# Optimization experiments

Measured on AMD Instinct MI355X. Metric: run time of the kernel, lower is better.

The kernel has to match this reference:

```python
import jax, jax.numpy as jnp
import numpy as np

DIM = 1536
HEADS = 8
DK = 64            # key_size
DV = DIM // HEADS  # value_size = 192
NPF = 32           # num_rel_pos_features
LN_EPS = 1e-3


def central_mask_features(positions, features, seq_len):
    # Borzoi/baskerville central-mask positional basis
    pow_rate = jnp.exp(jnp.log(seq_len + 1.0) / features)
    center_widths = pow_rate ** jnp.arange(1, features + 1, dtype=jnp.float32)
    return (center_widths[None, :] > jnp.abs(positions)[:, None]).astype(jnp.float32)


def get_positional_embed(n, feature_size):
    distances = jnp.arange(-n + 1, n, dtype=jnp.float32)  # (2n-1,)
    emb = central_mask_features(distances, feature_size // 2, n)
    return jnp.concatenate([emb, jnp.sign(distances)[:, None] * emb], axis=-1)  # (2n-1, F)


def relative_shift(x):
    # x: (b, h, n, 2n-1) -> (b, h, n, n), Transformer-XL shift trick
    b, h, t1, t2 = x.shape
    x = jnp.pad(x, ((0, 0), (0, 0), (0, 0), (1, 0)))  # (b,h,n,2n)
    x = x.reshape(b, h, t2 + 1, t1)[:, :, 1:, :]       # (b,h,2n-1,n)
    x = x.reshape(b, h, t1, t2)
    return x[..., :((t2 + 1) // 2)]


def setup_inputs() -> dict:
    key = jax.random.key(0)
    ks = jax.random.split(key, 10)
    s = 0.02
    return {
        "x": jax.random.normal(ks[0], (1, 4096, DIM), jnp.float32),
        "ln_gamma": jnp.ones((DIM,), jnp.float32),
        "ln_beta": jnp.zeros((DIM,), jnp.float32),
        "Wq": jax.random.normal(ks[1], (DIM, HEADS * DK), jnp.float32) * s,
        "Wk": jax.random.normal(ks[2], (DIM, HEADS * DK), jnp.float32) * s,
        "Wv": jax.random.normal(ks[3], (DIM, HEADS * DV), jnp.float32) * s,
        "Wr": jax.random.normal(ks[4], (NPF, HEADS * DK), jnp.float32) * s,
        "Wo": jax.random.normal(ks[5], (HEADS * DV, DIM), jnp.float32) * s,
        "bo": jnp.zeros((DIM,), jnp.float32),
        "rel_content_bias": jax.random.normal(ks[6], (1, HEADS, 1, DK), jnp.float32),
        "rel_pos_bias": jax.random.normal(ks[7], (1, HEADS, 1, DK), jnp.float32),
    }


def reference(x, ln_gamma, ln_beta, Wq, Wk, Wv, Wr, Wo, bo, rel_content_bias, rel_pos_bias):
    B, N, D = x.shape
    # LayerNorm(eps=1e-3)
    mu = jnp.mean(x, axis=-1, keepdims=True)
    var = jnp.mean(jnp.square(x - mu), axis=-1, keepdims=True)
    xn = (x - mu) * jax.lax.rsqrt(var + LN_EPS) * ln_gamma + ln_beta
    # projections -> (B,H,N,d)
    q = (xn @ Wq).reshape(B, N, HEADS, DK).transpose(0, 2, 1, 3) * (DK ** -0.5)
    k = (xn @ Wk).reshape(B, N, HEADS, DK).transpose(0, 2, 1, 3)
    v = (xn @ Wv).reshape(B, N, HEADS, DV).transpose(0, 2, 1, 3)
    content_logits = jnp.einsum('bhid,bhjd->bhij', q + rel_content_bias, k)
    # relative positions (dropout is identity in eval mode)
    pos = get_positional_embed(N, NPF)                       # (2N-1, NPF)
    rel_k = (pos @ Wr).reshape(2 * N - 1, HEADS, DK).transpose(1, 0, 2)  # (H,2N-1,DK)
    rel_logits = jnp.einsum('bhid,hjd->bhij', q + rel_pos_bias, rel_k)   # (B,H,N,2N-1)
    rel_logits = relative_shift(rel_logits)                  # (B,H,N,N)
    attn = jax.nn.softmax(content_logits + rel_logits, axis=-1)
    out = jnp.einsum('bhij,bhjd->bhid', attn, v)
    out = out.transpose(0, 2, 1, 3).reshape(B, N, HEADS * DV)
    return out @ Wo + bo
```

## Files before the change

### kernel.cpp

```cpp
#include <hip/hip_runtime.h>
#include <hip/hip_bf16.h>
#include <math.h>

typedef __hip_bfloat16 bf16;
typedef __attribute__((ext_vector_type(8))) short bf16x8;
typedef __attribute__((ext_vector_type(4))) float f32x4;

#define DIMX 1536
#define NSEQ 4096
#define NHEAD 8
#define DKH 64
#define DVH 192
#define HDK 512
#define HDV 1536
#define KSPLIT 2
#define KVB 32

static __device__ __forceinline__ float b2f(bf16 x){ return __bfloat162float(x); }
static __device__ __forceinline__ bf16 f2b(float x){ return __float2bfloat16(x); }

#define GLD_TO_LDS(gsrc, ldst) __builtin_amdgcn_global_load_lds( \
    (const __attribute__((address_space(1))) unsigned int*)(gsrc), \
    (__attribute__((address_space(3))) unsigned int*)(ldst), 16, 0, 0)

__global__ __launch_bounds__(256) void k_cvtT(const float* __restrict__ W, bf16* __restrict__ WT, int K, int N){
  __shared__ float t[32][33];
  int n0 = blockIdx.x<<5, k0 = blockIdx.y<<5;
  int tx = threadIdx.x & 31, ty = threadIdx.x >> 5;
  #pragma unroll
  for (int r=ty; r<32; r+=8) t[r][tx] = W[(size_t)(k0+r)*N + n0 + tx];
  __syncthreads();
  #pragma unroll
  for (int r=ty; r<32; r+=8) WT[(size_t)(n0+r)*K + k0 + tx] = f2b(t[tx][r]);
}

__global__ __launch_bounds__(256) void k_cvtT2(const float* __restrict__ W, bf16* __restrict__ WTh,
                                               bf16* __restrict__ WTl, int K, int N){
  __shared__ float t[32][33];
  int n0 = blockIdx.x<<5, k0 = blockIdx.y<<5;
  int tx = threadIdx.x & 31, ty = threadIdx.x >> 5;
  #pragma unroll
  for (int r=ty; r<32; r+=8) t[r][tx] = W[(size_t)(k0+r)*N + n0 + tx];
  __syncthreads();
  #pragma unroll
  for (int r=ty; r<32; r+=8){
    float v = t[tx][r];
    bf16 hi = f2b(v);
    WTh[(size_t)(n0+r)*K + k0 + tx] = hi;
    WTl[(size_t)(n0+r)*K + k0 + tx] = f2b(v - b2f(hi));
  }
}

__global__ __launch_bounds__(256) void k_T(const bf16* __restrict__ src, bf16* __restrict__ dst, int R, int C){
  __shared__ bf16 t[64][65];
  int c0 = blockIdx.x<<6, r0 = blockIdx.y<<6;
  int tx = threadIdx.x & 63, ty = threadIdx.x >> 6;
  for (int r=ty; r<64; r+=4) t[r][tx] = src[(size_t)(r0+r)*C + c0 + tx];
  __syncthreads();
  for (int r=ty; r<64; r+=4){
    int dv = c0+r, kv = r0+tx;
    int kvp = (kv & ~31) | ((((kv>>3)&3) ^ (dv&3))<<3) | (kv&7);
    dst[(size_t)dv*R + kvp] = t[tx][r];
  }
}

__global__ __launch_bounds__(256) void k_ln(const float* __restrict__ x, const float* __restrict__ g,
                                            const float* __restrict__ b,
                                            bf16* __restrict__ xnh, bf16* __restrict__ xnl){
  int row = blockIdx.x, t = threadIdx.x;
  const float* xr = x + (size_t)row*DIMX;
  float v[6]; float s=0.f, ss=0.f;
  #pragma unroll
  for (int j=0;j<6;++j){ v[j]=xr[t+256*j]; s+=v[j]; ss+=v[j]*v[j]; }
  int lane = t&63, wave = t>>6;
  #pragma unroll
  for (int off=32; off>0; off>>=1){ s += __shfl_down(s,off,64); ss += __shfl_down(ss,off,64); }
  __shared__ float red[8];
  if (lane==0){ red[wave]=s; red[wave+4]=ss; }
  __syncthreads();
  s = red[0]+red[1]+red[2]+red[3];
  ss = red[4]+red[5]+red[6]+red[7];
  float mu = s*(1.f/DIMX);
  float var = ss*(1.f/DIMX) - mu*mu;
  float rstd = rsqrtf(var + 1e-3f);
  #pragma unroll
  for (int j=0;j<6;++j){
    int c = t+256*j;
    float xv = (v[j]-mu)*rstd*g[c] + b[c];
    bf16 hi = f2b(xv);
    xnh[(size_t)row*DIMX + c] = hi;
    xnl[(size_t)row*DIMX + c] = f2b(xv - b2f(hi));
  }
}

template<int EPI>
__global__ __launch_bounds__(256) void k_gemm(const bf16* __restrict__ A, const bf16* __restrict__ BT,
    void* __restrict__ Cout, const float* __restrict__ bias, int M, int N, int K)
{
  __shared__ bf16 As[128][32];
  __shared__ bf16 Bs[128][32];
  int nbx = N>>7;
  int m0 = (blockIdx.x / nbx)<<7, n0 = (blockIdx.x % nbx)<<7;
  int tid = threadIdx.x, wave = tid>>6, lane = tid&63;
  int lr = lane&15, lc = lane>>4;
  int wm = (wave>>1)<<6, wn = (wave&1)<<6;
  f32x4 acc[4][4] = {};
  for (int k0=0; k0<K; k0+=32){
    __syncthreads();
    #pragma unroll
    for (int it=0; it<2; ++it){
      int id = tid + (it<<8);
      int rr = id>>2, cc = id&3;
      unsigned wbase = (unsigned)(((it<<8) + (tid & 192))*16);
      GLD_TO_LDS(A  + (size_t)(m0+rr)*K + k0 + cc*8, (char*)As + wbase);
      GLD_TO_LDS(BT + (size_t)(n0+rr)*K + k0 + cc*8, (char*)Bs + wbase);
    }
    __syncthreads();
    bf16x8 af[4], bfr[4];
    #pragma unroll
    for (int mt=0; mt<4; ++mt) af[mt] = *(const bf16x8*)(&As[wm + mt*16 + lr][lc*8]);
    #pragma unroll
    for (int nt=0; nt<4; ++nt) bfr[nt] = *(const bf16x8*)(&Bs[wn + nt*16 + lr][lc*8]);
    #pragma unroll
    for (int mt=0; mt<4; ++mt)
      #pragma unroll
      for (int nt=0; nt<4; ++nt)
        acc[mt][nt] = __builtin_amdgcn_mfma_f32_16x16x32_bf16(af[mt], bfr[nt], acc[mt][nt], 0,0,0);
  }
  #pragma unroll
  for (int mt=0; mt<4; ++mt){
    #pragma unroll
    for (int nt=0; nt<4; ++nt){
      #pragma unroll
      for (int reg=0; reg<4; ++reg){
        int row = m0 + wm + mt*16 + (lc<<2) + reg;
        int col = n0 + wn + nt*16 + lr;
        if (EPI==0) ((bf16*)Cout)[(size_t)row*N + col] = f2b(acc[mt][nt][reg]);
        else        ((float*)Cout)[(size_t)row*N + col] = acc[mt][nt][reg] + bias[col];
      }
    }
  }
}

template<int EPIQ>
__global__ __launch_bounds__(256) void k_gemm3(const bf16* __restrict__ Ahi, const bf16* __restrict__ Alo,
    const bf16* __restrict__ Bhi, const bf16* __restrict__ Blo,
    bf16* __restrict__ Ohi, bf16* __restrict__ Olo,
    const float* __restrict__ cb, int M, int N, int K)
{
  __shared__ bf16 Ash[128][32];
  __shared__ bf16 Asl[128][32];
  __shared__ bf16 Bsh[128][32];
  __shared__ bf16 Bsl[128][32];
  int nbx = N>>7;
  int m0 = (blockIdx.x / nbx)<<7, n0 = (blockIdx.x % nbx)<<7;
  int tid = threadIdx.x, wave = tid>>6, lane = tid&63;
  int lr = lane&15, lc = lane>>4;
  int wm = (wave>>1)<<6, wn = (wave&1)<<6;
  f32x4 acc[4][4] = {};
  for (int k0=0; k0<K; k0+=32){
    __syncthreads();
    #pragma unroll
    for (int it=0; it<2; ++it){
      int id = tid + (it<<8);
      int rr = id>>2, cc = id&3;
      unsigned wbase = (unsigned)(((it<<8) + (tid & 192))*16);
      size_t ga = (size_t)(m0+rr)*K + k0 + cc*8;
      size_t gb = (size_t)(n0+rr)*K + k0 + cc*8;
      GLD_TO_LDS(Ahi + ga, (char*)Ash + wbase);
      GLD_TO_LDS(Alo + ga, (char*)Asl + wbase);
      GLD_TO_LDS(Bhi + gb, (char*)Bsh + wbase);
      GLD_TO_LDS(Blo + gb, (char*)Bsl + wbase);
    }
    __syncthreads();
    bf16x8 ah[4], al[4], bh[4], bl[4];
    #pragma unroll
    for (int mt=0; mt<4; ++mt){
      ah[mt] = *(const bf16x8*)(&Ash[wm + mt*16 + lr][lc*8]);
      al[mt] = *(const bf16x8*)(&Asl[wm + mt*16 + lr][lc*8]);
    }
    #pragma unroll
    for (int nt=0; nt<4; ++nt){
      bh[nt] = *(const bf16x8*)(&Bsh[wn + nt*16 + lr][lc*8]);
      bl[nt] = *(const bf16x8*)(&Bsl[wn + nt*16 + lr][lc*8]);
    }
    #pragma unroll
    for (int mt=0; mt<4; ++mt)
      #pragma unroll
      for (int nt=0; nt<4; ++nt){
        acc[mt][nt] = __builtin_amdgcn_mfma_f32_16x16x32_bf16(ah[mt], bh[nt], acc[mt][nt], 0,0,0);
        acc[mt][nt] = __builtin_amdgcn_mfma_f32_16x16x32_bf16(al[mt], bh[nt], acc[mt][nt], 0,0,0);
        acc[mt][nt] = __builtin_amdgcn_mfma_f32_16x16x32_bf16(ah[mt], bl[nt], acc[mt][nt], 0,0,0);
      }
  }
  #pragma unroll
  for (int mt=0; mt<4; ++mt){
    #pragma unroll
    for (int nt=0; nt<4; ++nt){
      #pragma unroll
      for (int reg=0; reg<4; ++reg){
        int row = m0 + wm + mt*16 + (lc<<2) + reg;
        int col = n0 + wn + nt*16 + lr;
        float v = acc[mt][nt][reg];
        int colw = col;
        if (EPIQ==1) v = v*0.125f + cb[col & (HDK-1)];
        else colw = (col & ~63) | ((((col>>3)&7) ^ (row&7))<<3) | (col&7);
        bf16 hi = f2b(v);
        Ohi[(size_t)row*N + colw] = hi;
        Olo[(size_t)row*N + colw] = f2b(v - b2f(hi));
      }
    }
  }
}

__global__ __launch_bounds__(64) void k_abtab(const bf16* __restrict__ qph, const bf16* __restrict__ qpl,
                                              const float* __restrict__ Wr,
                                              const float* __restrict__ cb, const float* __restrict__ pb,
                                              float* __restrict__ ab){
  int i = blockIdx.x, h = blockIdx.y;
  int lane = threadIdx.x;
  __shared__ float qpp[64];
  __shared__ float us[32];
  size_t qi = (size_t)i*HDK + h*DKH + lane;
  int col = h*DKH + lane;
  qpp[lane] = b2f(qph[qi]) + b2f(qpl[qi]) - cb[col] + pb[col];
  __syncthreads();
  if (lane < 32){
    const float* wr = Wr + (size_t)lane*HDK + h*DKH;
    float u=0.f;
    #pragma unroll
    for (int d2=0; d2<64; ++d2) u += wr[d2]*qpp[d2];
    us[lane]=u;
  }
  __syncthreads();
  if (lane < 16){
    float a=0.f, bb=0.f;
    for (int f=15; f>=lane; --f){ a += us[f]; bb += us[16+f]; }
    float* o = ab + ((size_t)h*NSEQ + i)*32;
    o[lane]=a; o[16+lane]=bb;
  }
}

__global__ __launch_bounds__(256,4) void k_attn(
    const bf16* __restrict__ qph, const bf16* __restrict__ qpl,
    const bf16* __restrict__ khs, const bf16* __restrict__ kls,
    const bf16* __restrict__ vts, const float* __restrict__ ab,
    bf16* __restrict__ PO, float2* __restrict__ ML)
{
  int wg = blockIdx.x;
  int h  = wg & 7;
  int qtile = (wg >> 3) & 63;
  int ks = wg >> 9;
  int q0 = qtile * 64;
  int tid = threadIdx.x, wave = tid>>6, lane = tid&63;
  int lr = lane&15, lc = lane>>4;

  __shared__ bf16 Ksh[KVB][64];
  __shared__ bf16 Ksl[KVB][64];
  __shared__ bf16 Vs[DVH][KVB];
  __shared__ bf16 Ps[4][16][40];
  __shared__ float2 ABs[64][17];

  for (int xx=tid; xx<1024; xx+=256){
    int row = xx>>4, g = xx&15;
    const float* src = ab + ((size_t)h*NSEQ + q0 + row)*32;
    ABs[row][g] = make_float2(src[g], src[16+g]);
  }

  bf16x8 qfh[2], qfl[2];
  {
    int row = q0 + wave*16 + lr;
    const bf16* qrh = qph + (size_t)row*HDK + h*DKH;
    const bf16* qrl = qpl + (size_t)row*HDK + h*DKH;
    qfh[0] = *(const bf16x8*)(qrh + 8*lc);
    qfh[1] = *(const bf16x8*)(qrh + 32 + 8*lc);
    qfl[0] = *(const bf16x8*)(qrl + 8*lc);
    qfl[1] = *(const bf16x8*)(qrl + 32 + 8*lc);
  }
  const bf16* Kh = khs + h*DKH;
  const bf16* Kl = kls + h*DKH;
  const bf16* Vt = vts + (size_t)h*DVH*NSEQ;

  f32x4 oacc[12] = {};
  float mrow[4], lrow[4];
  #pragma unroll
  for (int r=0;r<4;++r){ mrow[r]=-3e38f; lrow[r]=0.f; }

  const float RCPL = 1.33329424f;
  int kv_lo = ks * (NSEQ/KSPLIT);
  int kv_hi = kv_lo + NSEQ/KSPLIT;

  for (int kv0=kv_lo; kv0<kv_hi; kv0+=KVB) {
    __syncthreads();
    {
      int r = tid>>3, c = tid&7;
      size_t gk = (size_t)(kv0+r)*HDK + c*8;
      GLD_TO_LDS(Kh + gk, (char*)Ksh + (tid&192)*16);
      GLD_TO_LDS(Kl + gk, (char*)Ksl + (tid&192)*16);
      #pragma unroll
      for (int j=0; j<3; ++j){
        int id = j*256 + tid;
        int vr = id>>2, vc = id&3;
        GLD_TO_LDS(Vt + (size_t)vr*NSEQ + kv0 + vc*8, (char*)Vs + (j*256 + (tid&192))*16);
      }
    }
    __syncthreads();

    f32x4 sf[2];
    #pragma unroll
    for (int ct=0; ct<2; ++ct){
      f32x4 s = {};
      int krow = ct*16 + lr;
      int sw0 = ((lc  ) ^ (krow&7))*8;
      int sw1 = ((lc+4) ^ (krow&7))*8;
      bf16x8 kh0 = *(const bf16x8*)(&Ksh[krow][sw0]);
      bf16x8 kh1 = *(const bf16x8*)(&Ksh[krow][sw1]);
      bf16x8 kl0 = *(const bf16x8*)(&Ksl[krow][sw0]);
      bf16x8 kl1 = *(const bf16x8*)(&Ksl[krow][sw1]);
      s = __builtin_amdgcn_mfma_f32_16x16x32_bf16(qfh[0], kh0, s, 0,0,0);
      s = __builtin_amdgcn_mfma_f32_16x16x32_bf16(qfh[1], kh1, s, 0,0,0);
      s = __builtin_amdgcn_mfma_f32_16x16x32_bf16(qfl[0], kh0, s, 0,0,0);
      s = __builtin_amdgcn_mfma_f32_16x16x32_bf16(qfl[1], kh1, s, 0,0,0);
      s = __builtin_amdgcn_mfma_f32_16x16x32_bf16(qfh[0], kl0, s, 0,0,0);
      s = __builtin_amdgcn_mfma_f32_16x16x32_bf16(qfh[1], kl1, s, 0,0,0);
      sf[ct]=s;
    }
    float mnew[4];
    #pragma unroll
    for (int r=0;r<4;++r) mnew[r]=mrow[r];
    #pragma unroll
    for (int ct=0; ct<2; ++ct){
      int j = kv0 + ct*16 + lr;
      #pragma unroll
      for (int reg=0; reg<4; ++reg){
        int rowloc = wave*16 + 4*lc + reg;
        int dd = j - (q0 + rowloc);
        int ad = dd<0 ? -dd : dd;
        int gg = ad ? (int)(__log2f((float)ad) * RCPL) : 0;
        float2 sb = ABs[rowloc][gg];
        float bias = sb.x + (dd>0 ? sb.y : (dd<0 ? -sb.y : 0.f));
        float sv = sf[ct][reg] + bias;
        sf[ct][reg] = sv;
        mnew[reg] = fmaxf(mnew[reg], sv);
      }
    }
    #pragma unroll
    for (int off=1; off<16; off<<=1){
      #pragma unroll
      for (int r=0;r<4;++r) mnew[r] = fmaxf(mnew[r], __shfl_xor(mnew[r], off, 64));
    }
    float scl[4];
    #pragma unroll
    for (int r=0;r<4;++r){
      scl[r] = __expf(mrow[r]-mnew[r]);
      mrow[r]=mnew[r];
      lrow[r]*=scl[r];
    }
    #pragma unroll
    for (int ct=0; ct<2; ++ct){
      #pragma unroll
      for (int reg=0; reg<4; ++reg){
        float p = __expf(sf[ct][reg]-mrow[reg]);
        lrow[reg]+=p;
        Ps[wave][4*lc+reg][ct*16+lr] = f2b(p);
      }
    }
    #pragma unroll
    for (int t12=0;t12<12;++t12){
      #pragma unroll
      for (int reg=0;reg<4;++reg) oacc[t12][reg]*=scl[reg];
    }
    bf16x8 pa = *(const bf16x8*)(&Ps[wave][lr][lc*8]);
    #pragma unroll
    for (int t12=0; t12<12; ++t12){
      int vrow = t12*16 + lr;
      bf16x8 v0 = *(const bf16x8*)(&Vs[vrow][(lc ^ (vrow&3))*8]);
      oacc[t12] = __builtin_amdgcn_mfma_f32_16x16x32_bf16(pa, v0, oacc[t12], 0,0,0);
    }
  }
  #pragma unroll
  for (int off=1; off<16; off<<=1){
    #pragma unroll
    for (int r=0;r<4;++r) lrow[r] += __shfl_xor(lrow[r], off, 64);
  }
  #pragma unroll
  for (int t12=0;t12<12;++t12){
    #pragma unroll
    for (int reg=0;reg<4;++reg){
      int rowloc = wave*16 + 4*lc + reg;
      PO[((size_t)wg*64 + rowloc)*DVH + t12*16 + lr] = f2b(oacc[t12][reg]);
    }
  }
  if (lr == 0){
    #pragma unroll
    for (int reg=0; reg<4; ++reg){
      int rowloc = wave*16 + 4*lc + reg;
      ML[(size_t)wg*64 + rowloc] = make_float2(mrow[reg], lrow[reg]);
    }
  }
}

__global__ __launch_bounds__(256) void k_comb(const bf16* __restrict__ PO, const float2* __restrict__ ML,
                                              bf16* __restrict__ Obuf){
  int i = blockIdx.x;
  int qtile = i>>6, rl = i&63;
  for (int c=threadIdx.x; c<HDV; c+=256){
    int h = c/DVH, d = c - h*DVH;
    int wg0 = qtile*8 + h, wg1 = 512 + wg0;
    float2 ml0 = ML[(size_t)wg0*64 + rl];
    float2 ml1 = ML[(size_t)wg1*64 + rl];
    float M = fmaxf(ml0.x, ml1.x);
    float w0 = __expf(ml0.x - M), w1 = __expf(ml1.x - M);
    float l = ml0.y*w0 + ml1.y*w1;
    float o = b2f(PO[((size_t)wg0*64 + rl)*DVH + d])*w0
            + b2f(PO[((size_t)wg1*64 + rl)*DVH + d])*w1;
    Obuf[(size_t)i*HDV + c] = f2b(o / l);
  }
}

extern "C" void kernel_launch(void* const* d_in, const int* in_sizes, int n_in,
                              void* d_out, int out_size, void* d_ws, size_t ws_size,
                              hipStream_t stream) {
  const float* x  = (const float*)d_in[0];
  const float* lg = (const float*)d_in[1];
  const float* lb = (const float*)d_in[2];
  const float* Wq = (const float*)d_in[3];
  const float* Wk = (const float*)d_in[4];
  const float* Wv = (const float*)d_in[5];
  const float* Wr = (const float*)d_in[6];
  const float* Wo = (const float*)d_in[7];
  const float* bo = (const float*)d_in[8];
  const float* cb = (const float*)d_in[9];
  const float* pb = (const float*)d_in[10];
  float* out = (float*)d_out;

  char* ws = (char*)d_ws;
  size_t off = 0;
  auto alloc = [&](size_t bytes)->void*{ void* p = ws + off; off += (bytes + 255) & ~(size_t)255; return p; };
  bf16* WoT  = (bf16*)alloc((size_t)DIMX*HDV*2);
  bf16* qph  = (bf16*)alloc((size_t)NSEQ*HDK*2);
  bf16* qpl  = (bf16*)alloc((size_t)NSEQ*HDK*2);
  bf16* kh   = (bf16*)alloc((size_t)NSEQ*HDK*2);
  bf16* kl   = (bf16*)alloc((size_t)NSEQ*HDK*2);
  bf16* vt   = (bf16*)alloc((size_t)HDV*NSEQ*2);
  float* ab  = (float*)alloc((size_t)NHEAD*NSEQ*32*4);
  bf16* Obuf = (bf16*)alloc((size_t)NSEQ*HDV*2);
  float2* ML = (float2*)alloc((size_t)KSPLIT*512*64*sizeof(float2));
  char* scratch = (char*)alloc(0);
  bf16* xnh  = (bf16*)alloc((size_t)NSEQ*DIMX*2);
  bf16* xnl  = (bf16*)alloc((size_t)NSEQ*DIMX*2);
  bf16* v_rm = (bf16*)alloc((size_t)NSEQ*HDV*2);
  bf16* WqTh = (bf16*)alloc((size_t)HDK*DIMX*2);
  bf16* WqTl = (bf16*)alloc((size_t)HDK*DIMX*2);
  bf16* WkTh = (bf16*)alloc((size_t)HDK*DIMX*2);
  bf16* WkTl = (bf16*)alloc((size_t)HDK*DIMX*2);
  bf16* WvT  = (bf16*)alloc((size_t)HDV*DIMX*2);
  bf16* PO   = (bf16*)scratch;
  (void)in_sizes; (void)n_in; (void)out_size; (void)ws_size;

  k_cvtT2<<<dim3(HDK/32,  DIMX/32), 256, 0, stream>>>(Wq, WqTh, WqTl, DIMX, HDK);
  k_cvtT2<<<dim3(HDK/32,  DIMX/32), 256, 0, stream>>>(Wk, WkTh, WkTl, DIMX, HDK);
  k_cvtT <<<dim3(HDV/32,  DIMX/32), 256, 0, stream>>>(Wv, WvT, DIMX, HDV);
  k_cvtT <<<dim3(DIMX/32, HDV/32),  256, 0, stream>>>(Wo, WoT, HDV, DIMX);
  k_ln<<<NSEQ, 256, 0, stream>>>(x, lg, lb, xnh, xnl);

  k_gemm3<1><<<(NSEQ/128)*(HDK/128), 256, 0, stream>>>(xnh, xnl, WqTh, WqTl, qph, qpl, cb, NSEQ, HDK, DIMX);
  k_gemm3<0><<<(NSEQ/128)*(HDK/128), 256, 0, stream>>>(xnh, xnl, WkTh, WkTl, kh, kl, nullptr, NSEQ, HDK, DIMX);
  k_gemm<0><<<(NSEQ/128)*(HDV/128), 256, 0, stream>>>(xnh, WvT, (void*)v_rm, nullptr, NSEQ, HDV, DIMX);

  k_abtab<<<dim3(NSEQ, NHEAD), 64, 0, stream>>>(qph, qpl, Wr, cb, pb, ab);
  k_T<<<dim3(HDV/64, NSEQ/64), 256, 0, stream>>>(v_rm, vt, NSEQ, HDV);

  k_attn<<<KSPLIT*512, 256, 0, stream>>>(qph, qpl, kh, kl, vt, ab, PO, ML);
  k_comb<<<NSEQ, 256, 0, stream>>>(PO, ML, Obuf);

  k_gemm<1><<<(NSEQ/128)*(DIMX/128), 256, 0, stream>>>(Obuf, WoT, (void*)out, bo, NSEQ, DIMX, HDV);
}
```

Measured before the change: 608.9 us.

## Drop weight low split, add XCD swizzle, lazy softmax rescale, fix LDS swizzles

Q and K projections now keep only the high bf16 part of the weights, which cuts one third of the MFMAs plus one LDS load stream per GEMM. GEMM blocks are remapped across XCDs for better L2 locality. The attention softmax rescales the output accumulators only when some row max grows by more than 8 in a wave, skipping the 48 multiplies per step otherwise. The V transpose and read swizzle changes to use row>>1, and the P buffer padding shrinks, both to reduce LDS bank conflicts. These add some precision loss in the projections and rely on the bounded stale max keeping exp values from overflowing.

Result: faster. 564.4 us (-7.3%).

```diff
diff --git a/kernel.cpp b/kernel.cpp
--- a/kernel.cpp
+++ b/kernel.cpp
@@ -23,6 +23,10 @@
     (const __attribute__((address_space(1))) unsigned int*)(gsrc), \
     (__attribute__((address_space(3))) unsigned int*)(ldst), 16, 0, 0)
 
+static __device__ __forceinline__ int xcd_swz(int b, int nwg){
+  return (b & 7)*(nwg>>3) + (b>>3);
+}
+
 __global__ __launch_bounds__(256) void k_cvtT(const float* __restrict__ W, bf16* __restrict__ WT, int K, int N){
   __shared__ float t[32][33];
   int n0 = blockIdx.x<<5, k0 = blockIdx.y<<5;
@@ -32,23 +36,6 @@
   __syncthreads();
   #pragma unroll
   for (int r=ty; r<32; r+=8) WT[(size_t)(n0+r)*K + k0 + tx] = f2b(t[tx][r]);
-}
-
-__global__ __launch_bounds__(256) void k_cvtT2(const float* __restrict__ W, bf16* __restrict__ WTh,
-                                               bf16* __restrict__ WTl, int K, int N){
-  __shared__ float t[32][33];
-  int n0 = blockIdx.x<<5, k0 = blockIdx.y<<5;
-  int tx = threadIdx.x & 31, ty = threadIdx.x >> 5;
-  #pragma unroll
-  for (int r=ty; r<32; r+=8) t[r][tx] = W[(size_t)(k0+r)*N + n0 + tx];
-  __syncthreads();
-  #pragma unroll
-  for (int r=ty; r<32; r+=8){
-    float v = t[tx][r];
-    bf16 hi = f2b(v);
-    WTh[(size_t)(n0+r)*K + k0 + tx] = hi;
-    WTl[(size_t)(n0+r)*K + k0 + tx] = f2b(v - b2f(hi));
-  }
 }
 
 __global__ __launch_bounds__(256) void k_T(const bf16* __restrict__ src, bf16* __restrict__ dst, int R, int C){
@@ -59,7 +46,7 @@
   __syncthreads();
   for (int r=ty; r<64; r+=4){
     int dv = c0+r, kv = r0+tx;
-    int kvp = (kv & ~31) | ((((kv>>3)&3) ^ (dv&3))<<3) | (kv&7);
+    int kvp = (kv & ~31) | ((((kv>>3)&3) ^ ((dv>>1)&3))<<3) | (kv&7);
     dst[(size_t)dv*R + kvp] = t[tx][r];
   }
 }
@@ -100,7 +87,8 @@
   __shared__ bf16 As[128][32];
   __shared__ bf16 Bs[128][32];
   int nbx = N>>7;
-  int m0 = (blockIdx.x / nbx)<<7, n0 = (blockIdx.x % nbx)<<7;
+  int bid = xcd_swz(blockIdx.x, gridDim.x);
+  int m0 = (bid / nbx)<<7, n0 = (bid % nbx)<<7;
   int tid = threadIdx.x, wave = tid>>6, lane = tid&63;
   int lr = lane&15, lc = lane>>4;
   int wm = (wave>>1)<<6, wn = (wave&1)<<6;
@@ -144,16 +132,16 @@
 
 template<int EPIQ>
 __global__ __launch_bounds__(256) void k_gemm3(const bf16* __restrict__ Ahi, const bf16* __restrict__ Alo,
-    const bf16* __restrict__ Bhi, const bf16* __restrict__ Blo,
+    const bf16* __restrict__ Bhi,
     bf16* __restrict__ Ohi, bf16* __restrict__ Olo,
     const float* __restrict__ cb, int M, int N, int K)
 {
   __shared__ bf16 Ash[128][32];
   __shared__ bf16 Asl[128][32];
   __shared__ bf16 Bsh[128][32];
-  __shared__ bf16 Bsl[128][32];
   int nbx = N>>7;
-  int m0 = (blockIdx.x / nbx)<<7, n0 = (blockIdx.x % nbx)<<7;
+  int bid = xcd_swz(blockIdx.x, gridDim.x);
+  int m0 = (bid / nbx)<<7, n0 = (bid % nbx)<<7;
   int tid = threadIdx.x, wave = tid>>6, lane = tid&63;
   int lr = lane&15, lc = lane>>4;
   int wm = (wave>>1)<<6, wn = (wave&1)<<6;
@@ -170,27 +158,23 @@
       GLD_TO_LDS(Ahi + ga, (char*)Ash + wbase);
       GLD_TO_LDS(Alo + ga, (char*)Asl + wbase);
       GLD_TO_LDS(Bhi + gb, (char*)Bsh + wbase);
-      GLD_TO_LDS(Blo + gb, (char*)Bsl + wbase);
-    }
-    __syncthreads();
-    bf16x8 ah[4], al[4], bh[4], bl[4];
+    }
+    __syncthreads();
+    bf16x8 ah[4], al[4], bh[4];
     #pragma unroll
     for (int mt=0; mt<4; ++mt){
       ah[mt] = *(const bf16x8*)(&Ash[wm + mt*16 + lr][lc*8]);
       al[mt] = *(const bf16x8*)(&Asl[wm + mt*16 + lr][lc*8]);
     }
     #pragma unroll
-    for (int nt=0; nt<4; ++nt){
+    for (int nt=0; nt<4; ++nt)
       bh[nt] = *(const bf16x8*)(&Bsh[wn + nt*16 + lr][lc*8]);
-      bl[nt] = *(const bf16x8*)(&Bsl[wn + nt*16 + lr][lc*8]);
-    }
     #pragma unroll
     for (int mt=0; mt<4; ++mt)
       #pragma unroll
       for (int nt=0; nt<4; ++nt){
         acc[mt][nt] = __builtin_amdgcn_mfma_f32_16x16x32_bf16(ah[mt], bh[nt], acc[mt][nt], 0,0,0);
         acc[mt][nt] = __builtin_amdgcn_mfma_f32_16x16x32_bf16(al[mt], bh[nt], acc[mt][nt], 0,0,0);
-        acc[mt][nt] = __builtin_amdgcn_mfma_f32_16x16x32_bf16(ah[mt], bl[nt], acc[mt][nt], 0,0,0);
       }
   }
   #pragma unroll
@@ -258,7 +242,7 @@
   __shared__ bf16 Ksh[KVB][64];
   __shared__ bf16 Ksl[KVB][64];
   __shared__ bf16 Vs[DVH][KVB];
-  __shared__ bf16 Ps[4][16][40];
+  __shared__ bf16 Ps[4][16][36];
   __shared__ float2 ABs[64][17];
 
   for (int xx=tid; xx<1024; xx+=256){
@@ -349,12 +333,22 @@
       #pragma unroll
       for (int r=0;r<4;++r) mnew[r] = fmaxf(mnew[r], __shfl_xor(mnew[r], off, 64));
     }
-    float scl[4];
-    #pragma unroll
-    for (int r=0;r<4;++r){
-      scl[r] = __expf(mrow[r]-mnew[r]);
-      mrow[r]=mnew[r];
-      lrow[r]*=scl[r];
+    bool okl = true;
+    #pragma unroll
+    for (int r=0;r<4;++r) okl = okl && (mnew[r] - mrow[r] <= 8.f);
+    if (!__all(okl)){
+      float scl[4];
+      #pragma unroll
+      for (int r=0;r<4;++r){
+        scl[r] = __expf(mrow[r]-mnew[r]);
+        mrow[r]=mnew[r];
+        lrow[r]*=scl[r];
+      }
+      #pragma unroll
+      for (int t12=0;t12<12;++t12){
+        #pragma unroll
+        for (int reg=0;reg<4;++reg) oacc[t12][reg]*=scl[reg];
+      }
     }
     #pragma unroll
     for (int ct=0; ct<2; ++ct){
@@ -365,16 +359,11 @@
         Ps[wave][4*lc+reg][ct*16+lr] = f2b(p);
       }
     }
-    #pragma unroll
-    for (int t12=0;t12<12;++t12){
-      #pragma unroll
-      for (int reg=0;reg<4;++reg) oacc[t12][reg]*=scl[reg];
-    }
     bf16x8 pa = *(const bf16x8*)(&Ps[wave][lr][lc*8]);
     #pragma unroll
     for (int t12=0; t12<12; ++t12){
       int vrow = t12*16 + lr;
-      bf16x8 v0 = *(const bf16x8*)(&Vs[vrow][(lc ^ (vrow&3))*8]);
+      bf16x8 v0 = *(const bf16x8*)(&Vs[vrow][(lc ^ ((vrow>>1)&3))*8]);
       oacc[t12] = __builtin_amdgcn_mfma_f32_16x16x32_bf16(pa, v0, oacc[t12], 0,0,0);
     }
   }
@@ -450,22 +439,20 @@
   bf16* xnh  = (bf16*)alloc((size_t)NSEQ*DIMX*2);
   bf16* xnl  = (bf16*)alloc((size_t)NSEQ*DIMX*2);
   bf16* v_rm = (bf16*)alloc((size_t)NSEQ*HDV*2);
-  bf16* WqTh = (bf16*)alloc((size_t)HDK*DIMX*2);
-  bf16* WqTl = (bf16*)alloc((size_t)HDK*DIMX*2);
-  bf16* WkTh = (bf16*)alloc((size_t)HDK*DIMX*2);
-  bf16* WkTl = (bf16*)alloc((size_t)HDK*DIMX*2);
+  bf16* WqT  = (bf16*)alloc((size_t)HDK*DIMX*2);
+  bf16* WkT  = (bf16*)alloc((size_t)HDK*DIMX*2);
   bf16* WvT  = (bf16*)alloc((size_t)HDV*DIMX*2);
   bf16* PO   = (bf16*)scratch;
   (void)in_sizes; (void)n_in; (void)out_size; (void)ws_size;
 
-  k_cvtT2<<<dim3(HDK/32,  DIMX/32), 256, 0, stream>>>(Wq, WqTh, WqTl, DIMX, HDK);
-  k_cvtT2<<<dim3(HDK/32,  DIMX/32), 256, 0, stream>>>(Wk, WkTh, WkTl, DIMX, HDK);
-  k_cvtT <<<dim3(HDV/32,  DIMX/32), 256, 0, stream>>>(Wv, WvT, DIMX, HDV);
-  k_cvtT <<<dim3(DIMX/32, HDV/32),  256, 0, stream>>>(Wo, WoT, HDV, DIMX);
+  k_cvtT<<<dim3(HDK/32,  DIMX/32), 256, 0, stream>>>(Wq, WqT, DIMX, HDK);
+  k_cvtT<<<dim3(HDK/32,  DIMX/32), 256, 0, stream>>>(Wk, WkT, DIMX, HDK);
+  k_cvtT<<<dim3(HDV/32,  DIMX/32), 256, 0, stream>>>(Wv, WvT, DIMX, HDV);
+  k_cvtT<<<dim3(DIMX/32, HDV/32),  256, 0, stream>>>(Wo, WoT, HDV, DIMX);
   k_ln<<<NSEQ, 256, 0, stream>>>(x, lg, lb, xnh, xnl);
 
-  k_gemm3<1><<<(NSEQ/128)*(HDK/128), 256, 0, stream>>>(xnh, xnl, WqTh, WqTl, qph, qpl, cb, NSEQ, HDK, DIMX);
-  k_gemm3<0><<<(NSEQ/128)*(HDK/128), 256, 0, stream>>>(xnh, xnl, WkTh, WkTl, kh, kl, nullptr, NSEQ, HDK, DIMX);
+  k_gemm3<1><<<(NSEQ/128)*(HDK/128), 256, 0, stream>>>(xnh, xnl, WqT, qph, qpl, cb, NSEQ, HDK, DIMX);
+  k_gemm3<0><<<(NSEQ/128)*(HDK/128), 256, 0, stream>>>(xnh, xnl, WkT, kh, kl, nullptr, NSEQ, HDK, DIMX);
   k_gemm<0><<<(NSEQ/128)*(HDV/128), 256, 0, stream>>>(xnh, WvT, (void*)v_rm, nullptr, NSEQ, HDV, DIMX);
 
   k_abtab<<<dim3(NSEQ, NHEAD), 64, 0, stream>>>(qph, qpl, Wr, cb, pb, ab);
```
